# Performance work log

Measured on AMD Instinct MI355X. Metric: run time of the kernel, lower is better.

The kernel has to match this reference:

```python
import jax, jax.numpy as jnp
import numpy as np

N_NODES = 100000
N_EDGES = 50000
NNZ = 1600000
C = 128
EPS = 0.0  # train_eps=False -> fixed buffer


def setup_inputs() -> dict:
    key = jax.random.key(0)
    k0, k1, k2, k3, k4 = jax.random.split(key, 5)
    x_0 = jax.random.normal(k0, (N_NODES, C), dtype=jnp.float32)
    node_idx = jax.random.randint(k1, (NNZ,), 0, N_NODES, dtype=jnp.int64)
    edge_idx = jax.random.randint(k2, (NNZ,), 0, N_EDGES, dtype=jnp.int64)
    # Linear(in_channels, in_channels) params (kaiming-uniform-ish scale)
    lim = 1.0 / np.sqrt(C)
    W = jax.random.uniform(k3, (C, C), minval=-lim, maxval=lim, dtype=jnp.float32)
    b = jax.random.uniform(k4, (C,), minval=-lim, maxval=lim, dtype=jnp.float32)
    return {"x_0": x_0, "node_idx": node_idx, "edge_idx": edge_idx, "W": W, "b": b}


def reference(x_0, node_idx, edge_idx, W, b):
    # Step 1: x_1 = B_1^T @ x_0  (hyperedge e sums features of its nodes)
    x_1 = jax.ops.segment_sum(x_0[node_idx], edge_idx, num_segments=N_EDGES)
    # Step 2: m_{1->0} = B_1 @ x_1 (node sums features of its incident hyperedges)
    m_1_0 = jax.ops.segment_sum(x_1[edge_idx], node_idx, num_segments=N_NODES)
    # Step 3: GIN update: Theta @ ((1+eps)*x_0 + m)
    out_0 = ((1.0 + EPS) * x_0 + m_1_0) @ W.T + b
    return (out_0, x_1)
```

## Files before the change

### kernel.cpp

```cpp
#include <hip/hip_runtime.h>
#include <stdint.h>

#define N_NODES 100000
#define N_EDGES 50000
#define C 128
#define NB 196
#define CAP 12288
#define X0_BLOCKS 25000
#define WBLOCKS 32
#define PCHUNK 8192

typedef short short8 __attribute__((ext_vector_type(8)));
typedef float f32x4  __attribute__((ext_vector_type(4)));

__device__ __forceinline__ unsigned int bf16rne(float f) {
    unsigned int u = __float_as_uint(f);
    return (u + 0x7FFFu + ((u >> 16) & 1u)) >> 16;
}
__device__ __forceinline__ unsigned int pk_bf16(float x, float y) {
    return (bf16rne(y) << 16) | bf16rne(x);
}
__device__ __forceinline__ float bf_lo(unsigned int u) { return __uint_as_float(u << 16); }
__device__ __forceinline__ float bf_hi(unsigned int u) { return __uint_as_float(u & 0xFFFF0000u); }

__global__ __launch_bounds__(256) void conv_hist(
    const float2* __restrict__ x0, const float2* __restrict__ W,
    unsigned int* __restrict__ x0h, unsigned int* __restrict__ Whu,
    const int* __restrict__ nidx, const int* __restrict__ eidx,
    int* __restrict__ Ceh, int* __restrict__ Cnh, int nnz)
{
    __shared__ int he[NB], hn[NB];
    int bid = blockIdx.x, t = threadIdx.x;
    if (bid < X0_BLOCKS) {
        int i = bid * 256 + t;
        float2 v = x0[i];
        x0h[i] = pk_bf16(v.x, v.y);
        return;
    }
    if (bid < X0_BLOCKS + WBLOCKS) {
        int i = (bid - X0_BLOCKS) * 256 + t;
        float2 v = W[i];
        Whu[i] = pk_bf16(v.x, v.y);
        return;
    }
    int chunk0 = (bid - X0_BLOCKS - WBLOCKS) * PCHUNK;
    for (int k = t; k < NB; k += 256) { he[k] = 0; hn[k] = 0; }
    __syncthreads();
#pragma unroll 4
    for (int j = 0; j < PCHUNK / 256; ++j) {
        int i = chunk0 + j * 256 + t;
        if (i < nnz) {
            atomicAdd(&he[eidx[i] >> 8], 1);
            atomicAdd(&hn[nidx[i] >> 9], 1);
        }
    }
    __syncthreads();
    for (int k = t; k < NB; k += 256) {
        if (he[k]) atomicAdd(&Ceh[k], he[k]);
        if (hn[k]) atomicAdd(&Cnh[k], hn[k]);
    }
}

__global__ __launch_bounds__(256) void coarse_scan(
    const int* __restrict__ Ceh, const int* __restrict__ Cnh,
    int* __restrict__ Cecur, int* __restrict__ Cncur)
{
    __shared__ int s[256];
    int t = threadIdx.x;
    int v = (t < NB) ? Ceh[t] : 0;
    s[t] = v; __syncthreads();
    for (int d = 1; d < 256; d <<= 1) {
        int u = (t >= d) ? s[t - d] : 0;
        __syncthreads(); s[t] += u; __syncthreads();
    }
    if (t < NB) Cecur[t] = s[t] - v;
    __syncthreads();
    v = (t < NB) ? Cnh[t] : 0;
    s[t] = v; __syncthreads();
    for (int d = 1; d < 256; d <<= 1) {
        int u = (t >= d) ? s[t - d] : 0;
        __syncthreads(); s[t] += u; __syncthreads();
    }
    if (t < NB) Cncur[t] = s[t] - v;
}

__global__ __launch_bounds__(256) void partition_kernel(
    const int* __restrict__ nidx, const int* __restrict__ eidx,
    int* __restrict__ Cecur, int* __restrict__ Cncur,
    unsigned int* __restrict__ pe, unsigned int* __restrict__ pn, int nnz)
{
    __shared__ int he[NB], hn[NB], be[NB], bn[NB];
    int t = threadIdx.x;
    int chunk0 = blockIdx.x * PCHUNK;
    for (int k = t; k < NB; k += 256) { he[k] = 0; hn[k] = 0; }
    __syncthreads();
#pragma unroll 4
    for (int j = 0; j < PCHUNK / 256; ++j) {
        int i = chunk0 + j * 256 + t;
        if (i < nnz) {
            atomicAdd(&he[eidx[i] >> 8], 1);
            atomicAdd(&hn[nidx[i] >> 9], 1);
        }
    }
    __syncthreads();
    for (int k = t; k < NB; k += 256) {
        be[k] = atomicAdd(&Cecur[k], he[k]);
        bn[k] = atomicAdd(&Cncur[k], hn[k]);
        he[k] = 0; hn[k] = 0;
    }
    __syncthreads();
#pragma unroll 4
    for (int j = 0; j < PCHUNK / 256; ++j) {
        int i = chunk0 + j * 256 + t;
        if (i < nnz) {
            int e = eidx[i], n = nidx[i];
            int re = atomicAdd(&he[e >> 8], 1);
            pe[be[e >> 8] + re] = (unsigned int)((e & 255) | (n << 8));
            int rn = atomicAdd(&hn[n >> 9], 1);
            pn[bn[n >> 9] + rn] = (unsigned int)((n & 511) | (e << 9));
        }
    }
}

__global__ __launch_bounds__(256) void bucket_scatter_ex(
    const unsigned int* __restrict__ pe, const unsigned int* __restrict__ pn,
    const int* __restrict__ Cecur, const int* __restrict__ Cncur,
    int* __restrict__ e_list, int* __restrict__ n_list,
    int* __restrict__ eoff, int* __restrict__ noff)
{
    __shared__ int cnt[512], cur[512], s[256];
    __shared__ int vals[CAP];
    bool eside = blockIdx.x < NB;
    int b = eside ? blockIdx.x : blockIdx.x - NB;
    const unsigned int* pairs = eside ? pe : pn;
    const int* endarr         = eside ? Cecur : Cncur;
    int* out                  = eside ? e_list : n_list;
    int* off                  = eside ? eoff : noff;
    int shift = eside ? 8 : 9;
    int mask  = (1 << shift) - 1;
    int kpb   = 1 << shift;
    int nkeys = eside ? N_EDGES : N_NODES;
    int key0 = b * kpb;
    int nk = nkeys - key0; if (nk > kpb) nk = kpb;
    if (nk <= 0) return;
    int start = (b == 0) ? 0 : endarr[b - 1];
    int end   = endarr[b];
    int t = threadIdx.x;

    for (int k = t; k < nk; k += 256) cnt[k] = 0;
    __syncthreads();
    for (int i = start + t; i < end; i += 256)
        atomicAdd(&cnt[(int)(pairs[i] & mask)], 1);
    __syncthreads();
    int k0 = 2 * t, k1 = 2 * t + 1;
    int c0 = (k0 < nk) ? cnt[k0] : 0;
    int c1 = (k1 < nk) ? cnt[k1] : 0;
    int local = c0 + c1;
    s[t] = local; __syncthreads();
    for (int d = 1; d < 256; d <<= 1) {
        int u = (t >= d) ? s[t - d] : 0;
        __syncthreads(); s[t] += u; __syncthreads();
    }
    int excl = s[t] - local;
    if (k0 < nk) { cur[k0] = excl;      off[key0 + k0] = start + excl; }
    if (k1 < nk) { cur[k1] = excl + c0; off[key0 + k1] = start + excl + c0; }
    if (b == NB - 1 && t == 0) off[nkeys] = end;
    __syncthreads();
    for (int i = start + t; i < end; i += 256) {
        unsigned int p = pairs[i];
        int key = (int)(p & mask);
        int val = (int)(p >> shift);
        int pos = atomicAdd(&cur[key], 1);
        if (pos < CAP) vals[pos] = val;
        else out[start + pos] = val;
    }
    __syncthreads();
    int sz = end - start; if (sz > CAP) sz = CAP;
    for (int j = t; j < sz; j += 256) out[start + j] = vals[j];
}

__device__ __forceinline__ float2 gather_bf16_rows(
    const unsigned int* __restrict__ src, const int* __restrict__ list,
    int s0, int s1, int lane)
{
    float ax0=0,ay0=0,ax1=0,ay1=0,ax2=0,ay2=0,ax3=0,ay3=0;
    float ax4=0,ay4=0,ax5=0,ay5=0,ax6=0,ay6=0,ax7=0,ay7=0;
    for (int base = s0; base < s1; base += 64) {
        int cnt = s1 - base; if (cnt > 64) cnt = 64;
        int my = (lane < cnt) ? list[base + lane] : 0;
        int j = 0;
        for (; j + 8 <= cnt; j += 8) {
            int g0 = __shfl(my, j+0), g1 = __shfl(my, j+1);
            int g2 = __shfl(my, j+2), g3 = __shfl(my, j+3);
            int g4 = __shfl(my, j+4), g5 = __shfl(my, j+5);
            int g6 = __shfl(my, j+6), g7 = __shfl(my, j+7);
            unsigned int u0 = src[(size_t)g0 * 64 + lane];
            unsigned int u1 = src[(size_t)g1 * 64 + lane];
            unsigned int u2 = src[(size_t)g2 * 64 + lane];
            unsigned int u3 = src[(size_t)g3 * 64 + lane];
            unsigned int u4 = src[(size_t)g4 * 64 + lane];
            unsigned int u5 = src[(size_t)g5 * 64 + lane];
            unsigned int u6 = src[(size_t)g6 * 64 + lane];
            unsigned int u7 = src[(size_t)g7 * 64 + lane];
            ax0 += bf_lo(u0); ay0 += bf_hi(u0);  ax1 += bf_lo(u1); ay1 += bf_hi(u1);
            ax2 += bf_lo(u2); ay2 += bf_hi(u2);  ax3 += bf_lo(u3); ay3 += bf_hi(u3);
            ax4 += bf_lo(u4); ay4 += bf_hi(u4);  ax5 += bf_lo(u5); ay5 += bf_hi(u5);
            ax6 += bf_lo(u6); ay6 += bf_hi(u6);  ax7 += bf_lo(u7); ay7 += bf_hi(u7);
        }
        for (; j < cnt; ++j) {
            int g = __shfl(my, j);
            unsigned int u = src[(size_t)g * 64 + lane];
            ax0 += bf_lo(u); ay0 += bf_hi(u);
        }
    }
    ax0+=ax1; ay0+=ay1; ax2+=ax3; ay2+=ay3; ax4+=ax5; ay4+=ay5; ax6+=ax7; ay6+=ay7;
    ax0+=ax2; ay0+=ay2; ax4+=ax6; ay4+=ay6;
    ax0+=ax4; ay0+=ay4;
    return make_float2(ax0, ay0);
}

__global__ __launch_bounds__(256) void seg_sum(
    const unsigned int* __restrict__ x0h, const int* __restrict__ list,
    const int* __restrict__ off, float2* __restrict__ x1,
    unsigned int* __restrict__ x1h, int nseg)
{
    int wid  = (blockIdx.x * 256 + threadIdx.x) >> 6;
    int lane = threadIdx.x & 63;
    if (wid >= nseg) return;
    float2 acc = gather_bf16_rows(x0h, list, off[wid], off[wid + 1], lane);
    x1 [(size_t)wid * 64 + lane] = acc;
    x1h[(size_t)wid * 64 + lane] = pk_bf16(acc.x, acc.y);
}

__global__ __launch_bounds__(256) void gin_fused(
    const unsigned int* __restrict__ x0h, const unsigned int* __restrict__ x1h,
    const int* __restrict__ n_list, const int* __restrict__ noff,
    const unsigned short* __restrict__ Wh, const float* __restrict__ b,
    float* __restrict__ out)
{
    __shared__ __align__(16) unsigned short ins[32][136];
    int t = threadIdx.x;
    int lane = t & 63, w = t >> 6;
    int row0 = blockIdx.x * 32;

    for (int r = w * 8; r < w * 8 + 8; ++r) {
        int node = row0 + r;
        unsigned int bu = x0h[(size_t)node * 64 + lane];
        float2 g = gather_bf16_rows(x1h, n_list, noff[node], noff[node + 1], lane);
        g.x += bf_lo(bu); g.y += bf_hi(bu);
        *(unsigned int*)&ins[r][lane * 2] = pk_bf16(g.x, g.y);
    }
    __syncthreads();

    int mt  = w & 1;
    int ntb = (w >> 1) * 4;
    int l15  = lane & 15;
    int koff = (lane >> 4) * 8;
    int arow = mt * 16 + l15;

    f32x4 acc0 = {0,0,0,0}, acc1 = {0,0,0,0}, acc2 = {0,0,0,0}, acc3 = {0,0,0,0};
#pragma unroll
    for (int kt = 0; kt < C; kt += 32) {
        short8 a = *(const short8*)&ins[arow][kt + koff];
        short8 b0 = *(const short8*)&Wh[(size_t)((ntb + 0) * 16 + l15) * C + kt + koff];
        short8 b1 = *(const short8*)&Wh[(size_t)((ntb + 1) * 16 + l15) * C + kt + koff];
        short8 b2 = *(const short8*)&Wh[(size_t)((ntb + 2) * 16 + l15) * C + kt + koff];
        short8 b3 = *(const short8*)&Wh[(size_t)((ntb + 3) * 16 + l15) * C + kt + koff];
        acc0 = __builtin_amdgcn_mfma_f32_16x16x32_bf16(a, b0, acc0, 0, 0, 0);
        acc1 = __builtin_amdgcn_mfma_f32_16x16x32_bf16(a, b1, acc1, 0, 0, 0);
        acc2 = __builtin_amdgcn_mfma_f32_16x16x32_bf16(a, b2, acc2, 0, 0, 0);
        acc3 = __builtin_amdgcn_mfma_f32_16x16x32_bf16(a, b3, acc3, 0, 0, 0);
    }

    int drow = row0 + mt * 16 + (lane >> 4) * 4;
#pragma unroll
    for (int n = 0; n < 4; ++n) {
        f32x4 accv = (n == 0) ? acc0 : (n == 1) ? acc1 : (n == 2) ? acc2 : acc3;
        int colg = (ntb + n) * 16 + l15;
        float bias = b[colg];
#pragma unroll
        for (int j = 0; j < 4; ++j)
            out[(size_t)(drow + j) * C + colg] = accv[j] + bias;
    }
}

__global__ __launch_bounds__(256) void scatter_rows(
    const float4* __restrict__ src, const int* __restrict__ gather_idx,
    const int* __restrict__ scatter_idx, float* __restrict__ dst, int nnz)
{
    int gid = blockIdx.x * 256 + threadIdx.x;
    int row = gid >> 5, lane = gid & 31;
    if (row >= nnz) return;
    float4 v = src[(size_t)gather_idx[row] * 32 + lane];
    float* d = dst + (size_t)scatter_idx[row] * C + lane * 4;
    atomicAdd(d + 0, v.x); atomicAdd(d + 1, v.y);
    atomicAdd(d + 2, v.z); atomicAdd(d + 3, v.w);
}

__global__ __launch_bounds__(256) void gin_gemm(
    const float* __restrict__ x0, const float* __restrict__ m,
    const float* __restrict__ W, const float* __restrict__ b,
    float* __restrict__ out)
{
    __shared__ float Ws[32][129];
    __shared__ float insf[32][33];
    int t = threadIdx.x;
    int col = t & 127, rg = t >> 7;
    int row0 = blockIdx.x * 32;
    float acc[16];
#pragma unroll
    for (int r = 0; r < 16; ++r) acc[r] = 0.f;
    float bias = b[col];
    for (int kt = 0; kt < C; kt += 32) {
#pragma unroll
        for (int j = 0; j < 16; ++j) {
            int i = j * 256 + t, wc = i >> 5, kl = i & 31;
            Ws[kl][wc] = W[(size_t)wc * C + kt + kl];
        }
#pragma unroll
        for (int j = 0; j < 4; ++j) {
            int i = j * 256 + t, r = i >> 5, kl = i & 31;
            size_t gi = (size_t)(row0 + r) * C + kt + kl;
            insf[r][kl] = x0[gi] + m[gi];
        }
        __syncthreads();
#pragma unroll
        for (int kl = 0; kl < 32; ++kl) {
            float wv = Ws[kl][col];
#pragma unroll
            for (int r = 0; r < 16; ++r)
                acc[r] += insf[rg * 16 + r][kl] * wv;
        }
        __syncthreads();
    }
#pragma unroll
    for (int r = 0; r < 16; ++r)
        out[(size_t)(row0 + rg * 16 + r) * C + col] = acc[r] + bias;
}

extern "C" void kernel_launch(void* const* d_in, const int* in_sizes, int n_in,
                              void* d_out, int out_size, void* d_ws, size_t ws_size,
                              hipStream_t stream) {
    const float* x0 = (const float*)d_in[0];
    const int* nidx = (const int*)d_in[1];
    const int* eidx = (const int*)d_in[2];
    const float* W  = (const float*)d_in[3];
    const float* b  = (const float*)d_in[4];

    float* out0 = (float*)d_out;
    float* x1   = out0 + (size_t)N_NODES * C;
    int nnz = in_sizes[1];

    auto align256 = [](char* q) {
        return (char*)(((uintptr_t)q + 255) & ~(uintptr_t)255);
    };
    char* p = align256((char*)d_ws);
    unsigned int* pe = (unsigned int*)p; p = align256(p + (size_t)nnz * 4);
    unsigned int* pn = (unsigned int*)p; p = align256(p + (size_t)nnz * 4);
    unsigned int* x0h = (unsigned int*)p; p = align256(p + (size_t)N_NODES * 64 * 4);
    unsigned int* x1h = (unsigned int*)p; p = align256(p + (size_t)N_EDGES * 64 * 4);
    int* e_list = (int*)p; p = align256(p + (size_t)nnz * 4);
    int* n_list = (int*)p; p = align256(p + (size_t)nnz * 4);
    int* eoff   = (int*)p; p = align256(p + (size_t)(N_EDGES + 1) * 4);
    int* noff   = (int*)p; p = align256(p + (size_t)(N_NODES + 1) * 4);
    int* Ceh    = (int*)p;
    int* Cnh    = Ceh + NB;
    p = align256((char*)(Cnh + NB));
    int* Cecur  = (int*)p; p = align256(p + NB * 4);
    int* Cncur  = (int*)p; p = align256(p + NB * 4);
    unsigned int* Whu = (unsigned int*)p; p = align256(p + (size_t)C * C / 2 * 4);
    size_t needed = (size_t)(p - (char*)d_ws);

    if (ws_size < needed) {
        float* m = (float*)d_ws;
        hipMemsetAsync(x1, 0, (size_t)N_EDGES * C * sizeof(float), stream);
        hipMemsetAsync(m,  0, (size_t)N_NODES * C * sizeof(float), stream);
        int blocks = (nnz + 7) / 8;
        scatter_rows<<<blocks, 256, 0, stream>>>((const float4*)x0, nidx, eidx, x1, nnz);
        scatter_rows<<<blocks, 256, 0, stream>>>((const float4*)x1, eidx, nidx, m, nnz);
        gin_gemm<<<N_NODES / 32, 256, 0, stream>>>(x0, m, W, b, out0);
        return;
    }

    int pblocks = (nnz + PCHUNK - 1) / PCHUNK;

    hipMemsetAsync(Ceh, 0, 2 * NB * sizeof(int), stream);
    conv_hist<<<X0_BLOCKS + WBLOCKS + pblocks, 256, 0, stream>>>(
        (const float2*)x0, (const float2*)W, x0h, Whu, nidx, eidx, Ceh, Cnh, nnz);

    coarse_scan<<<1, 256, 0, stream>>>(Ceh, Cnh, Cecur, Cncur);
    partition_kernel<<<pblocks, 256, 0, stream>>>(
        nidx, eidx, Cecur, Cncur, pe, pn, nnz);
    bucket_scatter_ex<<<2 * NB, 256, 0, stream>>>(
        pe, pn, Cecur, Cncur, e_list, n_list, eoff, noff);

    seg_sum<<<(N_EDGES * 64 + 255) / 256, 256, 0, stream>>>(
        x0h, e_list, eoff, (float2*)x1, x1h, N_EDGES);

    gin_fused<<<N_NODES / 32, 256, 0, stream>>>(
        x0h, x1h, n_list, noff,
        (const unsigned short*)Whu, b, out0);
}
```

Before: 252.9 us.

## Split fused gather+GEMM into separate gather kernel and MFMA GEMM kernel

Splits the fused node-gather plus GEMM kernel into two kernels. The first gathers hyperedge features per node and writes the bf16 sum in place over x0h. The second runs a standalone MFMA GEMM in which each wave computes a 16x128 tile, reading its A operand straight from global memory. The aim is better parallelism for the gather, with one wave per node instead of 8 serial rows per wave, at the cost of an extra global round trip of the intermediate and one more launch.

```diff
diff --git a/kernel.cpp b/kernel.cpp
--- a/kernel.cpp
+++ b/kernel.cpp
@@ -232,55 +232,52 @@
     x1h[(size_t)wid * 64 + lane] = pk_bf16(acc.x, acc.y);
 }
 
-__global__ __launch_bounds__(256) void gin_fused(
-    const unsigned int* __restrict__ x0h, const unsigned int* __restrict__ x1h,
-    const int* __restrict__ n_list, const int* __restrict__ noff,
+__global__ __launch_bounds__(256) void m_gather(
+    unsigned int* __restrict__ x0h, const unsigned int* __restrict__ x1h,
+    const int* __restrict__ n_list, const int* __restrict__ noff)
+{
+    int wid  = (blockIdx.x * 256 + threadIdx.x) >> 6;
+    int lane = threadIdx.x & 63;
+    if (wid >= N_NODES) return;
+    unsigned int bu = x0h[(size_t)wid * 64 + lane];
+    float2 g = gather_bf16_rows(x1h, n_list, noff[wid], noff[wid + 1], lane);
+    g.x += bf_lo(bu); g.y += bf_hi(bu);
+    x0h[(size_t)wid * 64 + lane] = pk_bf16(g.x, g.y);
+}
+
+__global__ __launch_bounds__(256) void gin_gemm_mfma(
+    const unsigned int* __restrict__ mh,
     const unsigned short* __restrict__ Wh, const float* __restrict__ b,
     float* __restrict__ out)
 {
-    __shared__ __align__(16) unsigned short ins[32][136];
     int t = threadIdx.x;
     int lane = t & 63, w = t >> 6;
-    int row0 = blockIdx.x * 32;
-
-    for (int r = w * 8; r < w * 8 + 8; ++r) {
-        int node = row0 + r;
-        unsigned int bu = x0h[(size_t)node * 64 + lane];
-        float2 g = gather_bf16_rows(x1h, n_list, noff[node], noff[node + 1], lane);
-        g.x += bf_lo(bu); g.y += bf_hi(bu);
-        *(unsigned int*)&ins[r][lane * 2] = pk_bf16(g.x, g.y);
-    }
-    __syncthreads();
-
-    int mt  = w & 1;
-    int ntb = (w >> 1) * 4;
+    int wrow0 = blockIdx.x * 64 + w * 16;
+    if (wrow0 >= N_NODES) return;
     int l15  = lane & 15;
     int koff = (lane >> 4) * 8;
-    int arow = mt * 16 + l15;
-
-    f32x4 acc0 = {0,0,0,0}, acc1 = {0,0,0,0}, acc2 = {0,0,0,0}, acc3 = {0,0,0,0};
+    const unsigned short* mrow = (const unsigned short*)mh + (size_t)(wrow0 + l15) * C;
+
+    f32x4 acc[8];
+#pragma unroll
+    for (int n = 0; n < 8; ++n) acc[n] = (f32x4){0, 0, 0, 0};
 #pragma unroll
     for (int kt = 0; kt < C; kt += 32) {
-        short8 a = *(const short8*)&ins[arow][kt + koff];
-        short8 b0 = *(const short8*)&Wh[(size_t)((ntb + 0) * 16 + l15) * C + kt + koff];
-        short8 b1 = *(const short8*)&Wh[(size_t)((ntb + 1) * 16 + l15) * C + kt + koff];
-        short8 b2 = *(const short8*)&Wh[(size_t)((ntb + 2) * 16 + l15) * C + kt + koff];
-        short8 b3 = *(const short8*)&Wh[(size_t)((ntb + 3) * 16 + l15) * C + kt + koff];
-        acc0 = __builtin_amdgcn_mfma_f32_16x16x32_bf16(a, b0, acc0, 0, 0, 0);
-        acc1 = __builtin_amdgcn_mfma_f32_16x16x32_bf16(a, b1, acc1, 0, 0, 0);
-        acc2 = __builtin_amdgcn_mfma_f32_16x16x32_bf16(a, b2, acc2, 0, 0, 0);
-        acc3 = __builtin_amdgcn_mfma_f32_16x16x32_bf16(a, b3, acc3, 0, 0, 0);
-    }
-
-    int drow = row0 + mt * 16 + (lane >> 4) * 4;
-#pragma unroll
-    for (int n = 0; n < 4; ++n) {
-        f32x4 accv = (n == 0) ? acc0 : (n == 1) ? acc1 : (n == 2) ? acc2 : acc3;
-        int colg = (ntb + n) * 16 + l15;
+        short8 a = *(const short8*)&mrow[kt + koff];
+#pragma unroll
+        for (int n = 0; n < 8; ++n) {
+            short8 bb = *(const short8*)&Wh[(size_t)(n * 16 + l15) * C + kt + koff];
+            acc[n] = __builtin_amdgcn_mfma_f32_16x16x32_bf16(a, bb, acc[n], 0, 0, 0);
+        }
+    }
+    int drow = wrow0 + (lane >> 4) * 4;
+#pragma unroll
+    for (int n = 0; n < 8; ++n) {
+        int colg = n * 16 + l15;
         float bias = b[colg];
 #pragma unroll
         for (int j = 0; j < 4; ++j)
-            out[(size_t)(drow + j) * C + colg] = accv[j] + bias;
+            out[(size_t)(drow + j) * C + colg] = acc[n][j] + bias;
     }
 }
 
@@ -397,7 +394,9 @@
     seg_sum<<<(N_EDGES * 64 + 255) / 256, 256, 0, stream>>>(
         x0h, e_list, eoff, (float2*)x1, x1h, N_EDGES);
 
-    gin_fused<<<N_NODES / 32, 256, 0, stream>>>(
-        x0h, x1h, n_list, noff,
-        (const unsigned short*)Whu, b, out0);
-}
+    m_gather<<<(N_NODES * 64 + 255) / 256, 256, 0, stream>>>(
+        x0h, x1h, n_list, noff);
+
+    gin_gemm_mfma<<<(N_NODES + 63) / 64, 256, 0, stream>>>(
+        x0h, (const unsigned short*)Whu, b, out0);
+}
```

Measured after the change: 245.4 us. 1.03x faster.
